# Optimization experiments

Hardware: AMD Instinct MI355X
Metric: run time of the kernel (lower is better)

The kernel has to match this reference:

```python
import jax, jax.numpy as jnp
import numpy as np

S = 8192   # sequence length (loop dim in original call())
D = 4096   # feature dim (last dim of G_M1/G_M2)


def setup_inputs() -> dict:
    key = jax.random.key(0)
    k1, k2, k3, k4 = jax.random.split(key, 4)
    return {
        "G_M1": jax.random.normal(k1, (S, D), dtype=jnp.float32),
        "G_M2": jax.random.normal(k2, (S, D), dtype=jnp.float32),
        "wp1": jax.random.normal(k3, (1, D), dtype=jnp.float32),
        "wp2": jax.random.normal(k4, (1, D), dtype=jnp.float32),
    }


def reference(G_M1, G_M2, wp1, wp2):
    # Original loop builds p = [wp . G_M[i] for i in range(S)] -> shape [1, S].
    # That is exactly a single GEMV: wp @ G_M^T.
    p1 = jnp.einsum("od,sd->os", wp1, G_M1)  # [1, S]
    p2 = jnp.einsum("od,sd->os", wp2, G_M2)  # [1, S]
    p1_pred = jax.nn.softmax(p1, axis=-1)
    p2_pred = jax.nn.softmax(p2, axis=-1)
    # tf.keras.backend.stack([p1, p2], axis=1) on two [1, S] -> [1, 2, S]
    return jnp.stack([p1_pred, p2_pred], axis=1)
```

## Files before the change

### kernel.cpp

```cpp
#include <hip/hip_runtime.h>

#define DD 4096
#define SS 8192

__global__ __launch_bounds__(256) void gemv_kernel(
    const float* __restrict__ G1, const float* __restrict__ G2,
    const float* __restrict__ wp1, const float* __restrict__ wp2,
    float* __restrict__ logits)
{
    const int wid  = threadIdx.x >> 6;
    const int lane = threadIdx.x & 63;
    const int rg   = blockIdx.x * 4 + wid;

    const float* G;
    const float* w;
    int row;
    if (rg < SS) { G = G1; w = wp1; row = rg; }
    else         { G = G2; w = wp2; row = rg - SS; }

    const float4* __restrict__ Grow = reinterpret_cast<const float4*>(G + (size_t)row * DD);
    const float4* __restrict__ W4   = reinterpret_cast<const float4*>(w);

    float acc = 0.f;
    #pragma unroll
    for (int i = 0; i < DD / 4 / 64; ++i) {
        float4 g  = Grow[i * 64 + lane];
        float4 ww = W4[i * 64 + lane];
        acc = fmaf(g.x, ww.x, acc);
        acc = fmaf(g.y, ww.y, acc);
        acc = fmaf(g.z, ww.z, acc);
        acc = fmaf(g.w, ww.w, acc);
    }

    #pragma unroll
    for (int off = 32; off > 0; off >>= 1)
        acc += __shfl_xor(acc, off, 64);

    if (lane == 0)
        logits[rg] = acc;
}

__global__ __launch_bounds__(1024) void softmax_kernel(
    const float* __restrict__ logits, float* __restrict__ out)
{
    const int r = blockIdx.x;
    const int t = threadIdx.x;
    const float* __restrict__ x = logits + (size_t)r * SS;

    float v[8];
    float m = -INFINITY;
    #pragma unroll
    for (int i = 0; i < 8; ++i) {
        v[i] = x[t + i * 1024];
        m = fmaxf(m, v[i]);
    }

    __shared__ float red[16];

    #pragma unroll
    for (int off = 32; off > 0; off >>= 1)
        m = fmaxf(m, __shfl_xor(m, off, 64));
    if ((t & 63) == 0) red[t >> 6] = m;
    __syncthreads();
    if (t < 64) {
        float mm = (t < 16) ? red[t] : -INFINITY;
        #pragma unroll
        for (int off = 8; off > 0; off >>= 1)
            mm = fmaxf(mm, __shfl_xor(mm, off, 64));
        if (t == 0) red[0] = mm;
    }
    __syncthreads();
    m = red[0];
    __syncthreads();

    float s = 0.f;
    #pragma unroll
    for (int i = 0; i < 8; ++i) {
        v[i] = expf(v[i] - m);
        s += v[i];
    }
    #pragma unroll
    for (int off = 32; off > 0; off >>= 1)
        s += __shfl_xor(s, off, 64);
    if ((t & 63) == 0) red[t >> 6] = s;
    __syncthreads();
    if (t < 64) {
        float ss = (t < 16) ? red[t] : 0.f;
        #pragma unroll
        for (int off = 8; off > 0; off >>= 1)
            ss += __shfl_xor(ss, off, 64);
        if (t == 0) red[0] = ss;
    }
    __syncthreads();
    const float inv = 1.0f / red[0];

    #pragma unroll
    for (int i = 0; i < 8; ++i)
        out[(size_t)r * SS + t + i * 1024] = v[i] * inv;
}

extern "C" void kernel_launch(void* const* d_in, const int* in_sizes, int n_in,
                              void* d_out, int out_size, void* d_ws, size_t ws_size,
                              hipStream_t stream) {
    const float* G1  = (const float*)d_in[0];
    const float* G2  = (const float*)d_in[1];
    const float* wp1 = (const float*)d_in[2];
    const float* wp2 = (const float*)d_in[3];
    float* out    = (float*)d_out;
    float* logits = (float*)d_ws;

    gemv_kernel<<<(2 * SS) / 4, 256, 0, stream>>>(G1, G2, wp1, wp2, logits);
    softmax_kernel<<<2, 1024, 0, stream>>>(logits, out);
}
```

Before: 277.8 us.

## Stage weight vector in LDS and process two rows per wave in GEMV

Each block now loads the 16KB weight vector into shared memory once and each wave computes two rows, reading weights from LDS instead of global/L2. The inner loop issues eight independent float4 loads per chunk with four separate accumulators to raise memory-level parallelism. Launch bounds request 8 blocks per CU, and the grid halves. This adds a syncthreads and an LDS staging cost per block, and a 16KB LDS footprint that can limit occupancy. The kernel is HBM-bound on 256MB of G reads, so any gain has to come from better load overlap.

```diff
diff --git a/kernel.cpp b/kernel.cpp
--- a/kernel.cpp
+++ b/kernel.cpp
@@ -2,42 +2,83 @@
 
 #define DD 4096
 #define SS 8192
+#define NRB 8
+#define NBLK ((2 * SS) / NRB)
 
-__global__ __launch_bounds__(256) void gemv_kernel(
+__global__ __launch_bounds__(256, 8) void gemv_kernel(
     const float* __restrict__ G1, const float* __restrict__ G2,
     const float* __restrict__ wp1, const float* __restrict__ wp2,
     float* __restrict__ logits)
 {
-    const int wid  = threadIdx.x >> 6;
-    const int lane = threadIdx.x & 63;
-    const int rg   = blockIdx.x * 4 + wid;
+    __shared__ float4 wlds[DD / 4];
 
-    const float* G;
-    const float* w;
-    int row;
-    if (rg < SS) { G = G1; w = wp1; row = rg; }
-    else         { G = G2; w = wp2; row = rg - SS; }
+    const int t   = threadIdx.x;
+    const int b   = blockIdx.x;
+    const int mat = b >> 10;
+    const int rb  = (b & 1023) * NRB;
 
-    const float4* __restrict__ Grow = reinterpret_cast<const float4*>(G + (size_t)row * DD);
-    const float4* __restrict__ W4   = reinterpret_cast<const float4*>(w);
-
-    float acc = 0.f;
-    #pragma unroll
-    for (int i = 0; i < DD / 4 / 64; ++i) {
-        float4 g  = Grow[i * 64 + lane];
-        float4 ww = W4[i * 64 + lane];
-        acc = fmaf(g.x, ww.x, acc);
-        acc = fmaf(g.y, ww.y, acc);
-        acc = fmaf(g.z, ww.z, acc);
-        acc = fmaf(g.w, ww.w, acc);
-    }
+    const float*  G  = mat ? G2 : G1;
+    const float4* W4 = reinterpret_cast<const float4*>(mat ? wp2 : wp1);
 
     #pragma unroll
-    for (int off = 32; off > 0; off >>= 1)
-        acc += __shfl_xor(acc, off, 64);
+    for (int k = 0; k < 4; ++k)
+        wlds[k * 256 + t] = W4[k * 256 + t];
+    __syncthreads();
 
-    if (lane == 0)
-        logits[rg] = acc;
+    const int wid  = t >> 6;
+    const int lane = t & 63;
+
+    #pragma unroll
+    for (int rr = 0; rr < 2; ++rr) {
+        const int row = rb + wid * 2 + rr;
+        const float4* __restrict__ Grow =
+            reinterpret_cast<const float4*>(G + (size_t)row * DD);
+
+        float a0 = 0.f, a1 = 0.f, a2 = 0.f, a3 = 0.f;
+        #pragma unroll
+        for (int c = 0; c < 2; ++c) {
+            float4 g0 = Grow[c * 512 +   0 + lane];
+            float4 g1 = Grow[c * 512 +  64 + lane];
+            float4 g2 = Grow[c * 512 + 128 + lane];
+            float4 g3 = Grow[c * 512 + 192 + lane];
+            float4 g4 = Grow[c * 512 + 256 + lane];
+            float4 g5 = Grow[c * 512 + 320 + lane];
+            float4 g6 = Grow[c * 512 + 384 + lane];
+            float4 g7 = Grow[c * 512 + 448 + lane];
+            float4 w0 = wlds[c * 512 +   0 + lane];
+            float4 w1 = wlds[c * 512 +  64 + lane];
+            float4 w2 = wlds[c * 512 + 128 + lane];
+            float4 w3 = wlds[c * 512 + 192 + lane];
+            float4 w4 = wlds[c * 512 + 256 + lane];
+            float4 w5 = wlds[c * 512 + 320 + lane];
+            float4 w6 = wlds[c * 512 + 384 + lane];
+            float4 w7 = wlds[c * 512 + 448 + lane];
+            a0 = fmaf(g0.x, w0.x, a0); a0 = fmaf(g0.y, w0.y, a0);
+            a0 = fmaf(g0.z, w0.z, a0); a0 = fmaf(g0.w, w0.w, a0);
+            a1 = fmaf(g1.x, w1.x, a1); a1 = fmaf(g1.y, w1.y, a1);
+            a1 = fmaf(g1.z, w1.z, a1); a1 = fmaf(g1.w, w1.w, a1);
+            a2 = fmaf(g2.x, w2.x, a2); a2 = fmaf(g2.y, w2.y, a2);
+            a2 = fmaf(g2.z, w2.z, a2); a2 = fmaf(g2.w, w2.w, a2);
+            a3 = fmaf(g3.x, w3.x, a3); a3 = fmaf(g3.y, w3.y, a3);
+            a3 = fmaf(g3.z, w3.z, a3); a3 = fmaf(g3.w, w3.w, a3);
+            a0 = fmaf(g4.x, w4.x, a0); a0 = fmaf(g4.y, w4.y, a0);
+            a0 = fmaf(g4.z, w4.z, a0); a0 = fmaf(g4.w, w4.w, a0);
+            a1 = fmaf(g5.x, w5.x, a1); a1 = fmaf(g5.y, w5.y, a1);
+            a1 = fmaf(g5.z, w5.z, a1); a1 = fmaf(g5.w, w5.w, a1);
+            a2 = fmaf(g6.x, w6.x, a2); a2 = fmaf(g6.y, w6.y, a2);
+            a2 = fmaf(g6.z, w6.z, a2); a2 = fmaf(g6.w, w6.w, a2);
+            a3 = fmaf(g7.x, w7.x, a3); a3 = fmaf(g7.y, w7.y, a3);
+            a3 = fmaf(g7.z, w7.z, a3); a3 = fmaf(g7.w, w7.w, a3);
+        }
+        float acc = (a0 + a1) + (a2 + a3);
+
+        #pragma unroll
+        for (int off = 32; off > 0; off >>= 1)
+            acc += __shfl_xor(acc, off, 64);
+
+        if (lane == 0)
+            logits[mat * SS + row] = acc;
+    }
 }
 
 __global__ __launch_bounds__(1024) void softmax_kernel(
@@ -109,6 +150,6 @@
     float* out    = (float*)d_out;
     float* logits = (float*)d_ws;
 
-    gemv_kernel<<<(2 * SS) / 4, 256, 0, stream>>>(G1, G2, wp1, wp2, logits);
+    gemv_kernel<<<NBLK, 256, 0, stream>>>(G1, G2, wp1, wp2, logits);
     softmax_kernel<<<2, 1024, 0, stream>>>(logits, out);
 }
```

After: 280.0 us. No clear change (+0.8%).
